# Kernel tuning notes

Measured on AMD Instinct MI355X. Metric: run time of the kernel, lower is better.

## Reference

```python
import jax, jax.numpy as jnp
import numpy as np
import math

B, S, D, DFF = 32, 2048, 512, 512


def setup_inputs() -> dict:
    key = jax.random.key(0)
    ks = jax.random.split(key, 10)
    s = 1.0 / math.sqrt(D)
    inp = {
        "x": jax.random.normal(ks[0], (B, S, D), dtype=jnp.float32),
        "Wq": jax.random.uniform(ks[1], (DFF, D), jnp.float32, -s, s),
        "bq": jax.random.uniform(ks[2], (DFF,), jnp.float32, -s, s),
        "Wk": jax.random.uniform(ks[3], (DFF, D), jnp.float32, -s, s),
        "bk": jax.random.uniform(ks[4], (DFF,), jnp.float32, -s, s),
        "Wv": jax.random.uniform(ks[5], (DFF, D), jnp.float32, -s, s),
        "bv": jax.random.uniform(ks[6], (DFF,), jnp.float32, -s, s),
        "Wt": jax.random.uniform(ks[7], (1, S), jnp.float32, -1.0 / math.sqrt(S), 1.0 / math.sqrt(S)),
        "bt": jax.random.uniform(ks[8], (1,), jnp.float32, -1.0 / math.sqrt(S), 1.0 / math.sqrt(S)),
    }
    return inp


def reference(x, Wq, bq, Wk, bk, Wv, bv, Wt, bt):
    # QKV projections: [B,S,DFF]
    q = jnp.einsum('bsd,fd->bsf', x, Wq) + bq
    k = jnp.einsum('bsd,fd->bsf', x, Wk) + bk
    v = jnp.einsum('bsd,fd->bsf', x, Wv) + bv
    # attention scores: [B,S,S]
    scores = jnp.einsum('bsf,btf->bst', q, k) / math.sqrt(DFF)
    # temporal reduction Linear(S->1): [B,S,1] -> [B,S]
    ta = jnp.einsum('bst,t->bs', scores, Wt[0]) + bt[0]
    # V-weighted sum: [B,DFF]
    latent = jnp.einsum('bsf,bs->bf', v, ta)
    return latent
```

## Files before the change

### kernel.cpp

```cpp
#include <hip/hip_runtime.h>

#define NB 32
#define NS 2048
#define ND 512
#define NFF 512
#define SCALE 0.044194173824159216f

#define CPB 64
#define ROWS 32

__device__ __forceinline__ float dot4(float4 a, float4 b) {
    return a.x * b.x + a.y * b.y + a.z * b.z + a.w * b.w;
}

__device__ __forceinline__ float wave_reduce(float p) {
#pragma unroll
    for (int m = 1; m < 64; m <<= 1) p += __shfl_xor(p, m, 64);
    return p;
}

__global__ void __launch_bounds__(256) k_xw(const float* __restrict__ x,
                                            const float* __restrict__ Wt,
                                            float* __restrict__ xwp) {
    const int b = blockIdx.x >> 6;
    const int chunk = blockIdx.x & 63;
    const int s0 = chunk * ROWS;
    const int t = threadIdx.x;
    const int col = t & 127;
    const int half = t >> 7;
    const float4* xb = (const float4*)(x + (size_t)b * NS * ND);
    float4 acc = make_float4(0.f, 0.f, 0.f, 0.f);
#pragma unroll 4
    for (int i = 0; i < 16; i++) {
        int s = s0 + half + 2 * i;
        float w = Wt[s];
        float4 v = xb[(size_t)s * 128 + col];
        acc.x += w * v.x; acc.y += w * v.y; acc.z += w * v.z; acc.w += w * v.w;
    }
    __shared__ float4 red[128];
    if (half == 1) red[col] = acc;
    __syncthreads();
    if (half == 0) {
        float4 o = red[col];
        o.x += acc.x; o.y += acc.y; o.z += acc.z; o.w += acc.w;
        ((float4*)xwp)[(size_t)blockIdx.x * 128 + col] = o;
    }
}

__global__ void __launch_bounds__(256) k_kw(const float* __restrict__ xwp,
                                            const float* __restrict__ Wt,
                                            const float* __restrict__ Wk,
                                            const float* __restrict__ bk,
                                            const float* __restrict__ bq,
                                            float* __restrict__ kw,
                                            float* __restrict__ kwbq) {
    const int b = blockIdx.x >> 3;
    const int f0 = (blockIdx.x & 7) * 64;
    const int t = threadIdx.x;
    const int wv = t >> 6;
    const int lane = t & 63;
    __shared__ float sA[ND];
    __shared__ float sW[4];
    __shared__ float swt_s;
    {
        float a0 = 0.f, a1 = 0.f;
        const float* p = xwp + (size_t)b * CPB * ND + t;
#pragma unroll 8
        for (int c = 0; c < CPB; c++) {
            a0 += p[(size_t)c * ND];
            a1 += p[(size_t)c * ND + 256];
        }
        sA[t] = a0;
        sA[256 + t] = a1;
    }
    if (wv == 0) {
        float a = 0.f;
#pragma unroll
        for (int j = 0; j < 32; j++) a += Wt[j * 64 + lane];
        a = wave_reduce(a);
        if (lane == 0) swt_s = a;
    }
    __syncthreads();
    const float4* xw4 = (const float4*)sA;
    const float4 xa = xw4[lane];
    const float4 xc = xw4[64 + lane];
    const float sw = swt_s;
    float cbp = 0.f;
#pragma unroll 4
    for (int j = 0; j < 16; j++) {
        int f = f0 + wv * 16 + j;
        const float4* wr = (const float4*)(Wk + (size_t)f * ND);
        float pd = dot4(xa, wr[lane]) + dot4(xc, wr[64 + lane]);
        pd = wave_reduce(pd);
        if (lane == 0) {
            float kf = pd + bk[f] * sw;
            kw[b * NFF + f] = kf;
            cbp += kf * bq[f];
        }
    }
    if (lane == 0) sW[wv] = cbp;
    __syncthreads();
    if (t == 0) kwbq[blockIdx.x] = sW[0] + sW[1] + sW[2] + sW[3];
}

__global__ void __launch_bounds__(256) k_wqs(const float* __restrict__ kw,
                                             const float* __restrict__ Wq,
                                             const float* __restrict__ kwbq,
                                             const float* __restrict__ bt,
                                             float* __restrict__ wqs,
                                             float* __restrict__ cb2) {
    const int b = blockIdx.x >> 2;
    const int d0 = (blockIdx.x & 3) * 128;
    const int t = threadIdx.x;
    const int dl = t & 127;
    const int h = t >> 7;
    __shared__ float part[2][128];
    float acc = 0.f;
    const float* kwb = kw + b * NFF + h * 256;
    const float* wq = Wq + (size_t)h * 256 * ND + d0 + dl;
#pragma unroll 8
    for (int j = 0; j < 256; j++) acc += kwb[j] * wq[(size_t)j * ND];
    part[h][dl] = acc;
    __syncthreads();
    if (h == 0) wqs[b * ND + d0 + dl] = SCALE * (part[0][dl] + part[1][dl]);
    if ((blockIdx.x & 3) == 0 && t == 0) {
        float s = 0.f;
#pragma unroll
        for (int k = 0; k < 8; k++) s += kwbq[b * 8 + k];
        cb2[b] = SCALE * s + bt[0];
    }
}

__global__ void __launch_bounds__(256) k_ta_xt(const float* __restrict__ x,
                                               const float* __restrict__ wqs,
                                               const float* __restrict__ cb2,
                                               float* __restrict__ xtp,
                                               float* __restrict__ stp) {
    const int b = blockIdx.x >> 6;
    const int chunk = blockIdx.x & 63;
    const int wv = threadIdx.x >> 6;
    const int lane = threadIdx.x & 63;
    const float4* xb = (const float4*)(x + (size_t)b * NS * ND);
    const float4* wq4 = (const float4*)(wqs + b * ND);
    const float4 w0 = wq4[lane];
    const float4 w1 = wq4[64 + lane];
    const float c = cb2[b];
    float4 a0 = make_float4(0.f, 0.f, 0.f, 0.f);
    float4 a1 = make_float4(0.f, 0.f, 0.f, 0.f);
    float sta = 0.f;
#pragma unroll 2
    for (int i = 0; i < 8; i++) {
        int s = chunk * ROWS + wv * 8 + i;
        float4 v0 = xb[(size_t)s * 128 + lane];
        float4 v1 = xb[(size_t)s * 128 + 64 + lane];
        float pd = dot4(v0, w0) + dot4(v1, w1);
        pd = wave_reduce(pd);
        float ta = pd + c;
        a0.x += ta * v0.x; a0.y += ta * v0.y; a0.z += ta * v0.z; a0.w += ta * v0.w;
        a1.x += ta * v1.x; a1.y += ta * v1.y; a1.z += ta * v1.z; a1.w += ta * v1.w;
        sta += ta;
    }
    __shared__ float4 sh0[4][64];
    __shared__ float4 sh1[4][64];
    __shared__ float sW[4];
    sh0[wv][lane] = a0;
    sh1[wv][lane] = a1;
    if (lane == 0) sW[wv] = sta;
    __syncthreads();
    const int t = threadIdx.x;
    float4* dst = (float4*)xtp + (size_t)blockIdx.x * 128;
    if (t < 64) {
        float4 s0 = sh0[0][t], s1 = sh0[1][t], s2 = sh0[2][t], s3 = sh0[3][t];
        dst[t] = make_float4(s0.x + s1.x + s2.x + s3.x,
                             s0.y + s1.y + s2.y + s3.y,
                             s0.z + s1.z + s2.z + s3.z,
                             s0.w + s1.w + s2.w + s3.w);
    } else if (t < 128) {
        int l = t - 64;
        float4 s0 = sh1[0][l], s1 = sh1[1][l], s2 = sh1[2][l], s3 = sh1[3][l];
        dst[64 + l] = make_float4(s0.x + s1.x + s2.x + s3.x,
                                  s0.y + s1.y + s2.y + s3.y,
                                  s0.z + s1.z + s2.z + s3.z,
                                  s0.w + s1.w + s2.w + s3.w);
    } else if (t == 128) {
        stp[blockIdx.x] = sW[0] + sW[1] + sW[2] + sW[3];
    }
}

__global__ void __launch_bounds__(256) k_latent(const float* __restrict__ xtp,
                                                const float* __restrict__ stp,
                                                const float* __restrict__ Wv,
                                                const float* __restrict__ bv,
                                                float* __restrict__ out) {
    const int b = blockIdx.x >> 3;
    const int f0 = (blockIdx.x & 7) * 64;
    const int t = threadIdx.x;
    const int wv = t >> 6;
    const int lane = t & 63;
    __shared__ float sA[ND];
    __shared__ float sts;
    {
        float a0 = 0.f, a1 = 0.f;
        const float* p = xtp + (size_t)b * CPB * ND + t;
#pragma unroll 8
        for (int c = 0; c < CPB; c++) {
            a0 += p[(size_t)c * ND];
            a1 += p[(size_t)c * ND + 256];
        }
        sA[t] = a0;
        sA[256 + t] = a1;
        if (t == 0) {
            float s = 0.f;
            const float* sp = stp + b * CPB;
#pragma unroll
            for (int c = 0; c < CPB; c++) s += sp[c];
            sts = s;
        }
    }
    __syncthreads();
    const float4* xt4 = (const float4*)sA;
    const float4 xa = xt4[lane];
    const float4 xc = xt4[64 + lane];
    const float stb = sts;
#pragma unroll 4
    for (int j = 0; j < 16; j++) {
        int f = f0 + wv * 16 + j;
        const float4* wr = (const float4*)(Wv + (size_t)f * ND);
        float pd = dot4(xa, wr[lane]) + dot4(xc, wr[64 + lane]);
        pd = wave_reduce(pd);
        if (lane == 0) out[b * NFF + f] = pd + bv[f] * stb;
    }
}

extern "C" void kernel_launch(void* const* d_in, const int* in_sizes, int n_in,
                              void* d_out, int out_size, void* d_ws, size_t ws_size,
                              hipStream_t stream) {
    const float* x  = (const float*)d_in[0];
    const float* Wq = (const float*)d_in[1];
    const float* bq = (const float*)d_in[2];
    const float* Wk = (const float*)d_in[3];
    const float* bk = (const float*)d_in[4];
    const float* Wv = (const float*)d_in[5];
    const float* bv = (const float*)d_in[6];
    const float* Wt = (const float*)d_in[7];
    const float* bt = (const float*)d_in[8];
    float* out = (float*)d_out;

    float* w = (float*)d_ws;
    float* xwp  = w;
    float* xtp  = w + 1048576;
    float* stp  = w + 2097152;
    float* kw   = w + 2099200;
    float* kwbq = w + 2115584;
    float* wqs  = w + 2115840;
    float* cb2  = w + 2132224;

    k_xw<<<NB * CPB, 256, 0, stream>>>(x, Wt, xwp);
    k_kw<<<256, 256, 0, stream>>>(xwp, Wt, Wk, bk, bq, kw, kwbq);
    k_wqs<<<128, 256, 0, stream>>>(kw, Wq, kwbq, bt, wqs, cb2);
    k_ta_xt<<<NB * CPB, 256, 0, stream>>>(x, wqs, cb2, xtp, stp);
    k_latent<<<256, 256, 0, stream>>>(xtp, stp, Wv, bv, out);
}
```

Before: 280.7 us.

## Fuse five kernels into two passes with atomic reduction and last-block tail

Merges the x-weighted reduction with the Wk/Wq projections, and the attention-weighted reduction with the Wv projection, into two kernels. Per-chunk partials are accumulated with float atomics into per-batch buffers, and the last block per batch, detected via an atomic counter, performs the small GEMV tail. This removes three launches and the partial-sum buffers, but concentrates each batch's tail work in a single block and adds atomic contention and a memset.

```diff
diff --git a/kernel.cpp b/kernel.cpp
--- a/kernel.cpp
+++ b/kernel.cpp
@@ -19,60 +19,65 @@
     return p;
 }
 
-__global__ void __launch_bounds__(256) k_xw(const float* __restrict__ x,
-                                            const float* __restrict__ Wt,
-                                            float* __restrict__ xwp) {
+__global__ void __launch_bounds__(256)
+k_pass1(const float* __restrict__ x, const float* __restrict__ Wt,
+        const float* __restrict__ Wk, const float* __restrict__ bk,
+        const float* __restrict__ Wq, const float* __restrict__ bq,
+        const float* __restrict__ bt,
+        float* __restrict__ xw, float* __restrict__ wqs,
+        float* __restrict__ cb2, int* __restrict__ cnt1) {
     const int b = blockIdx.x >> 6;
     const int chunk = blockIdx.x & 63;
-    const int s0 = chunk * ROWS;
     const int t = threadIdx.x;
     const int col = t & 127;
     const int half = t >> 7;
     const float4* xb = (const float4*)(x + (size_t)b * NS * ND);
-    float4 acc = make_float4(0.f, 0.f, 0.f, 0.f);
+
+    {
+        const int s0 = chunk * ROWS;
+        float4 acc = make_float4(0.f, 0.f, 0.f, 0.f);
 #pragma unroll 4
-    for (int i = 0; i < 16; i++) {
-        int s = s0 + half + 2 * i;
-        float w = Wt[s];
-        float4 v = xb[(size_t)s * 128 + col];
-        acc.x += w * v.x; acc.y += w * v.y; acc.z += w * v.z; acc.w += w * v.w;
-    }
-    __shared__ float4 red[128];
-    if (half == 1) red[col] = acc;
-    __syncthreads();
-    if (half == 0) {
-        float4 o = red[col];
-        o.x += acc.x; o.y += acc.y; o.z += acc.z; o.w += acc.w;
-        ((float4*)xwp)[(size_t)blockIdx.x * 128 + col] = o;
-    }
-}
-
-__global__ void __launch_bounds__(256) k_kw(const float* __restrict__ xwp,
-                                            const float* __restrict__ Wt,
-                                            const float* __restrict__ Wk,
-                                            const float* __restrict__ bk,
-                                            const float* __restrict__ bq,
-                                            float* __restrict__ kw,
-                                            float* __restrict__ kwbq) {
-    const int b = blockIdx.x >> 3;
-    const int f0 = (blockIdx.x & 7) * 64;
-    const int t = threadIdx.x;
+        for (int i = 0; i < 16; i++) {
+            int s = s0 + half + 2 * i;
+            float w = Wt[s];
+            float4 v = xb[(size_t)s * 128 + col];
+            acc.x += w * v.x; acc.y += w * v.y; acc.z += w * v.z; acc.w += w * v.w;
+        }
+        __shared__ float4 red[128];
+        if (half == 1) red[col] = acc;
+        __syncthreads();
+        if (half == 0) {
+            float4 o = red[col];
+            float* dst = xw + b * ND + 4 * col;
+            atomicAdd(dst + 0, acc.x + o.x);
+            atomicAdd(dst + 1, acc.y + o.y);
+            atomicAdd(dst + 2, acc.z + o.z);
+            atomicAdd(dst + 3, acc.w + o.w);
+        }
+    }
+    __syncthreads();
+
+    __shared__ int lastFlag;
+    if (t == 0) {
+        int old = __hip_atomic_fetch_add(&cnt1[b], 1, __ATOMIC_ACQ_REL,
+                                         __HIP_MEMORY_SCOPE_AGENT);
+        lastFlag = (old == CPB - 1);
+    }
+    __syncthreads();
+    if (!lastFlag) return;
+    __threadfence();
+
     const int wv = t >> 6;
     const int lane = t & 63;
     __shared__ float sA[ND];
-    __shared__ float sW[4];
+    __shared__ float kwl[NFF];
+    __shared__ float cbred[4];
     __shared__ float swt_s;
-    {
-        float a0 = 0.f, a1 = 0.f;
-        const float* p = xwp + (size_t)b * CPB * ND + t;
-#pragma unroll 8
-        for (int c = 0; c < CPB; c++) {
-            a0 += p[(size_t)c * ND];
-            a1 += p[(size_t)c * ND + 256];
-        }
-        sA[t] = a0;
-        sA[256 + t] = a1;
-    }
+
+    sA[t] = __hip_atomic_load(&xw[b * ND + t], __ATOMIC_RELAXED,
+                              __HIP_MEMORY_SCOPE_AGENT);
+    sA[256 + t] = __hip_atomic_load(&xw[b * ND + 256 + t], __ATOMIC_RELAXED,
+                                    __HIP_MEMORY_SCOPE_AGENT);
     if (wv == 0) {
         float a = 0.f;
 #pragma unroll
@@ -81,154 +86,139 @@
         if (lane == 0) swt_s = a;
     }
     __syncthreads();
-    const float4* xw4 = (const float4*)sA;
-    const float4 xa = xw4[lane];
-    const float4 xc = xw4[64 + lane];
-    const float sw = swt_s;
-    float cbp = 0.f;
+
+    {
+        const float4* xw4 = (const float4*)sA;
+        const float4 xa = xw4[lane];
+        const float4 xc = xw4[64 + lane];
+        const float sw = swt_s;
+        float cbp = 0.f;
 #pragma unroll 4
-    for (int j = 0; j < 16; j++) {
-        int f = f0 + wv * 16 + j;
-        const float4* wr = (const float4*)(Wk + (size_t)f * ND);
-        float pd = dot4(xa, wr[lane]) + dot4(xc, wr[64 + lane]);
-        pd = wave_reduce(pd);
-        if (lane == 0) {
-            float kf = pd + bk[f] * sw;
-            kw[b * NFF + f] = kf;
-            cbp += kf * bq[f];
-        }
-    }
-    if (lane == 0) sW[wv] = cbp;
-    __syncthreads();
-    if (t == 0) kwbq[blockIdx.x] = sW[0] + sW[1] + sW[2] + sW[3];
-}
-
-__global__ void __launch_bounds__(256) k_wqs(const float* __restrict__ kw,
-                                             const float* __restrict__ Wq,
-                                             const float* __restrict__ kwbq,
-                                             const float* __restrict__ bt,
-                                             float* __restrict__ wqs,
-                                             float* __restrict__ cb2) {
-    const int b = blockIdx.x >> 2;
-    const int d0 = (blockIdx.x & 3) * 128;
-    const int t = threadIdx.x;
-    const int dl = t & 127;
-    const int h = t >> 7;
-    __shared__ float part[2][128];
-    float acc = 0.f;
-    const float* kwb = kw + b * NFF + h * 256;
-    const float* wq = Wq + (size_t)h * 256 * ND + d0 + dl;
+        for (int j = 0; j < 128; j++) {
+            int f = wv * 128 + j;
+            const float4* wr = (const float4*)(Wk + (size_t)f * ND);
+            float pd = dot4(xa, wr[lane]) + dot4(xc, wr[64 + lane]);
+            pd = wave_reduce(pd);
+            if (lane == 0) {
+                float kf = pd + bk[f] * sw;
+                kwl[f] = kf;
+                cbp += kf * bq[f];
+            }
+        }
+        if (lane == 0) cbred[wv] = cbp;
+    }
+    __syncthreads();
+
+    {
+        float a0 = 0.f, a1 = 0.f;
 #pragma unroll 8
-    for (int j = 0; j < 256; j++) acc += kwb[j] * wq[(size_t)j * ND];
-    part[h][dl] = acc;
-    __syncthreads();
-    if (h == 0) wqs[b * ND + d0 + dl] = SCALE * (part[0][dl] + part[1][dl]);
-    if ((blockIdx.x & 3) == 0 && t == 0) {
-        float s = 0.f;
-#pragma unroll
-        for (int k = 0; k < 8; k++) s += kwbq[b * 8 + k];
-        cb2[b] = SCALE * s + bt[0];
-    }
-}
-
-__global__ void __launch_bounds__(256) k_ta_xt(const float* __restrict__ x,
-                                               const float* __restrict__ wqs,
-                                               const float* __restrict__ cb2,
-                                               float* __restrict__ xtp,
-                                               float* __restrict__ stp) {
+        for (int f = 0; f < NFF; f++) {
+            float kf = kwl[f];
+            const float* wr = Wq + (size_t)f * ND;
+            a0 += kf * wr[t];
+            a1 += kf * wr[256 + t];
+        }
+        wqs[b * ND + t] = SCALE * a0;
+        wqs[b * ND + 256 + t] = SCALE * a1;
+        if (t == 0)
+            cb2[b] = SCALE * (cbred[0] + cbred[1] + cbred[2] + cbred[3]) + bt[0];
+    }
+}
+
+__global__ void __launch_bounds__(256)
+k_pass2(const float* __restrict__ x, const float* __restrict__ wqs,
+        const float* __restrict__ cb2, const float* __restrict__ Wv,
+        const float* __restrict__ bv,
+        float* __restrict__ xt, float* __restrict__ st,
+        float* __restrict__ out, int* __restrict__ cnt2) {
     const int b = blockIdx.x >> 6;
     const int chunk = blockIdx.x & 63;
     const int wv = threadIdx.x >> 6;
     const int lane = threadIdx.x & 63;
+    const int t = threadIdx.x;
     const float4* xb = (const float4*)(x + (size_t)b * NS * ND);
-    const float4* wq4 = (const float4*)(wqs + b * ND);
-    const float4 w0 = wq4[lane];
-    const float4 w1 = wq4[64 + lane];
-    const float c = cb2[b];
-    float4 a0 = make_float4(0.f, 0.f, 0.f, 0.f);
-    float4 a1 = make_float4(0.f, 0.f, 0.f, 0.f);
-    float sta = 0.f;
+
+    {
+        const float4* wq4 = (const float4*)(wqs + b * ND);
+        const float4 w0 = wq4[lane];
+        const float4 w1 = wq4[64 + lane];
+        const float c = cb2[b];
+        float4 a0 = make_float4(0.f, 0.f, 0.f, 0.f);
+        float4 a1 = make_float4(0.f, 0.f, 0.f, 0.f);
+        float sta = 0.f;
 #pragma unroll 2
-    for (int i = 0; i < 8; i++) {
-        int s = chunk * ROWS + wv * 8 + i;
-        float4 v0 = xb[(size_t)s * 128 + lane];
-        float4 v1 = xb[(size_t)s * 128 + 64 + lane];
-        float pd = dot4(v0, w0) + dot4(v1, w1);
-        pd = wave_reduce(pd);
-        float ta = pd + c;
-        a0.x += ta * v0.x; a0.y += ta * v0.y; a0.z += ta * v0.z; a0.w += ta * v0.w;
-        a1.x += ta * v1.x; a1.y += ta * v1.y; a1.z += ta * v1.z; a1.w += ta * v1.w;
-        sta += ta;
-    }
-    __shared__ float4 sh0[4][64];
-    __shared__ float4 sh1[4][64];
-    __shared__ float sW[4];
-    sh0[wv][lane] = a0;
-    sh1[wv][lane] = a1;
-    if (lane == 0) sW[wv] = sta;
-    __syncthreads();
-    const int t = threadIdx.x;
-    float4* dst = (float4*)xtp + (size_t)blockIdx.x * 128;
-    if (t < 64) {
-        float4 s0 = sh0[0][t], s1 = sh0[1][t], s2 = sh0[2][t], s3 = sh0[3][t];
-        dst[t] = make_float4(s0.x + s1.x + s2.x + s3.x,
-                             s0.y + s1.y + s2.y + s3.y,
-                             s0.z + s1.z + s2.z + s3.z,
-                             s0.w + s1.w + s2.w + s3.w);
-    } else if (t < 128) {
-        int l = t - 64;
-        float4 s0 = sh1[0][l], s1 = sh1[1][l], s2 = sh1[2][l], s3 = sh1[3][l];
-        dst[64 + l] = make_float4(s0.x + s1.x + s2.x + s3.x,
-                                  s0.y + s1.y + s2.y + s3.y,
-                                  s0.z + s1.z + s2.z + s3.z,
-                                  s0.w + s1.w + s2.w + s3.w);
-    } else if (t == 128) {
-        stp[blockIdx.x] = sW[0] + sW[1] + sW[2] + sW[3];
-    }
-}
-
-__global__ void __launch_bounds__(256) k_latent(const float* __restrict__ xtp,
-                                                const float* __restrict__ stp,
-                                                const float* __restrict__ Wv,
-                                                const float* __restrict__ bv,
-                                                float* __restrict__ out) {
-    const int b = blockIdx.x >> 3;
-    const int f0 = (blockIdx.x & 7) * 64;
-    const int t = threadIdx.x;
-    const int wv = t >> 6;
-    const int lane = t & 63;
+        for (int i = 0; i < 8; i++) {
+            int s = chunk * ROWS + wv * 8 + i;
+            float4 v0 = xb[(size_t)s * 128 + lane];
+            float4 v1 = xb[(size_t)s * 128 + 64 + lane];
+            float pd = dot4(v0, w0) + dot4(v1, w1);
+            pd = wave_reduce(pd);
+            float ta = pd + c;
+            a0.x += ta * v0.x; a0.y += ta * v0.y; a0.z += ta * v0.z; a0.w += ta * v0.w;
+            a1.x += ta * v1.x; a1.y += ta * v1.y; a1.z += ta * v1.z; a1.w += ta * v1.w;
+            sta += ta;
+        }
+        __shared__ float4 sh0[4][64];
+        __shared__ float4 sh1[4][64];
+        __shared__ float sW[4];
+        sh0[wv][lane] = a0;
+        sh1[wv][lane] = a1;
+        if (lane == 0) sW[wv] = sta;
+        __syncthreads();
+        if (t < 64) {
+            float4 s0 = sh0[0][t], s1 = sh0[1][t], s2 = sh0[2][t], s3 = sh0[3][t];
+            float* dst = xt + b * ND + 4 * t;
+            atomicAdd(dst + 0, s0.x + s1.x + s2.x + s3.x);
+            atomicAdd(dst + 1, s0.y + s1.y + s2.y + s3.y);
+            atomicAdd(dst + 2, s0.z + s1.z + s2.z + s3.z);
+            atomicAdd(dst + 3, s0.w + s1.w + s2.w + s3.w);
+        } else if (t < 128) {
+            int l = t - 64;
+            float4 s0 = sh1[0][l], s1 = sh1[1][l], s2 = sh1[2][l], s3 = sh1[3][l];
+            float* dst = xt + b * ND + 256 + 4 * l;
+            atomicAdd(dst + 0, s0.x + s1.x + s2.x + s3.x);
+            atomicAdd(dst + 1, s0.y + s1.y + s2.y + s3.y);
+            atomicAdd(dst + 2, s0.z + s1.z + s2.z + s3.z);
+            atomicAdd(dst + 3, s0.w + s1.w + s2.w + s3.w);
+        } else if (t == 128) {
+            atomicAdd(st + b, sW[0] + sW[1] + sW[2] + sW[3]);
+        }
+    }
+    __syncthreads();
+
+    __shared__ int lastFlag;
+    if (t == 0) {
+        int old = __hip_atomic_fetch_add(&cnt2[b], 1, __ATOMIC_ACQ_REL,
+                                         __HIP_MEMORY_SCOPE_AGENT);
+        lastFlag = (old == CPB - 1);
+    }
+    __syncthreads();
+    if (!lastFlag) return;
+    __threadfence();
+
     __shared__ float sA[ND];
-    __shared__ float sts;
-    {
-        float a0 = 0.f, a1 = 0.f;
-        const float* p = xtp + (size_t)b * CPB * ND + t;
-#pragma unroll 8
-        for (int c = 0; c < CPB; c++) {
-            a0 += p[(size_t)c * ND];
-            a1 += p[(size_t)c * ND + 256];
-        }
-        sA[t] = a0;
-        sA[256 + t] = a1;
-        if (t == 0) {
-            float s = 0.f;
-            const float* sp = stp + b * CPB;
-#pragma unroll
-            for (int c = 0; c < CPB; c++) s += sp[c];
-            sts = s;
-        }
-    }
-    __syncthreads();
-    const float4* xt4 = (const float4*)sA;
-    const float4 xa = xt4[lane];
-    const float4 xc = xt4[64 + lane];
-    const float stb = sts;
+    __shared__ float sScalar;
+    sA[t] = __hip_atomic_load(&xt[b * ND + t], __ATOMIC_RELAXED,
+                              __HIP_MEMORY_SCOPE_AGENT);
+    sA[256 + t] = __hip_atomic_load(&xt[b * ND + 256 + t], __ATOMIC_RELAXED,
+                                    __HIP_MEMORY_SCOPE_AGENT);
+    if (t == 0)
+        sScalar = __hip_atomic_load(&st[b], __ATOMIC_RELAXED,
+                                    __HIP_MEMORY_SCOPE_AGENT);
+    __syncthreads();
+    {
+        const float4* xt4 = (const float4*)sA;
+        const float4 xa = xt4[lane];
+        const float4 xc = xt4[64 + lane];
+        const float stb = sScalar;
 #pragma unroll 4
-    for (int j = 0; j < 16; j++) {
-        int f = f0 + wv * 16 + j;
-        const float4* wr = (const float4*)(Wv + (size_t)f * ND);
-        float pd = dot4(xa, wr[lane]) + dot4(xc, wr[64 + lane]);
-        pd = wave_reduce(pd);
-        if (lane == 0) out[b * NFF + f] = pd + bv[f] * stb;
+        for (int j = 0; j < 128; j++) {
+            int f = wv * 128 + j;
+            const float4* wr = (const float4*)(Wv + (size_t)f * ND);
+            float pd = dot4(xa, wr[lane]) + dot4(xc, wr[64 + lane]);
+            pd = wave_reduce(pd);
+            if (lane == 0) out[b * NFF + f] = pd + bv[f] * stb;
+        }
     }
 }
 
@@ -247,17 +237,18 @@
     float* out = (float*)d_out;
 
     float* w = (float*)d_ws;
-    float* xwp  = w;
-    float* xtp  = w + 1048576;
-    float* stp  = w + 2097152;
-    float* kw   = w + 2099200;
-    float* kwbq = w + 2115584;
-    float* wqs  = w + 2115840;
-    float* cb2  = w + 2132224;
-
-    k_xw<<<NB * CPB, 256, 0, stream>>>(x, Wt, xwp);
-    k_kw<<<256, 256, 0, stream>>>(xwp, Wt, Wk, bk, bq, kw, kwbq);
-    k_wqs<<<128, 256, 0, stream>>>(kw, Wq, kwbq, bt, wqs, cb2);
-    k_ta_xt<<<NB * CPB, 256, 0, stream>>>(x, wqs, cb2, xtp, stp);
-    k_latent<<<256, 256, 0, stream>>>(xtp, stp, Wv, bv, out);
-}
+    float* xw   = w;
+    float* xt   = w + 16384;
+    float* st   = w + 32768;
+    int*   cnt1 = (int*)(w + 32800);
+    int*   cnt2 = (int*)(w + 32832);
+    float* wqs  = w + 32864;
+    float* cb2  = w + 49248;
+
+    hipMemsetAsync(d_ws, 0, (size_t)32864 * sizeof(float), stream);
+
+    k_pass1<<<NB * CPB, 256, 0, stream>>>(x, Wt, Wk, bk, Wq, bq, bt,
+                                          xw, wqs, cb2, cnt1);
+    k_pass2<<<NB * CPB, 256, 0, stream>>>(x, wqs, cb2, Wv, bv,
+                                          xt, st, out, cnt2);
+}
```

Result: slower. 659.2 us (+134.8%).
